# Performance work log

Hardware: AMD Instinct MI355X
Metric: run time of the kernel (lower is better)

Reference implementation:

```python
import jax, jax.numpy as jnp
from jax import lax
import numpy as np

EPS = 1e-5
K = 9  # 3x3 kernel points


def conv2d(x, w, b, pad, mode):
    if pad > 0:
        x = jnp.pad(x, ((0, 0), (0, 0), (pad, pad), (pad, pad)), mode=mode)
    y = lax.conv_general_dilated(x, w, (1, 1), 'VALID',
                                 dimension_numbers=('NCHW', 'OIHW', 'NCHW'))
    return y + b[None, :, None, None]


def inorm(x):
    m = jnp.mean(x, axis=(2, 3), keepdims=True)
    v = jnp.var(x, axis=(2, 3), keepdims=True)
    return (x - m) * lax.rsqrt(v + EPS)


def upsample2(x):
    return jnp.repeat(jnp.repeat(x, 2, axis=2), 2, axis=3)


def resblock(x, w1, b1, w2, b2):
    h = jax.nn.relu(inorm(conv2d(x, w1, b1, 1, 'reflect')))
    return x + inorm(conv2d(h, w2, b2, 1, 'reflect'))


def mod_deform_conv(feat, cat_in, w_off, b_off, w, b):
    # ModulatedDeformConvPack(double=True): offsets+mask predicted from cat_in
    # (2C channels), deformable 3x3 conv applied to feat (C channels).
    B, C, H, W = feat.shape
    om = conv2d(cat_in, w_off, b_off, 1, 'constant')          # [B, 3K, H, W]
    dy, dx = om[:, :K], om[:, K:2 * K]
    mask = jax.nn.sigmoid(om[:, 2 * K:])                       # [B, K, H, W]
    offset = jnp.concatenate([dy, dx], axis=1)                 # [B, 2K, H, W]
    ky = (jnp.arange(K) // 3 - 1).astype(feat.dtype)
    kx = (jnp.arange(K) % 3 - 1).astype(feat.dtype)
    py = jnp.arange(H, dtype=feat.dtype)[None, None, :, None] + ky[None, :, None, None] + dy
    px = jnp.arange(W, dtype=feat.dtype)[None, None, None, :] + kx[None, :, None, None] + dx
    y0 = jnp.floor(py); x0 = jnp.floor(px)
    wy = py - y0; wx = px - x0
    feat_flat = feat.reshape(B, C, H * W)

    def corner(yi, xi, wt):
        valid = (yi >= 0) & (yi < H) & (xi >= 0) & (xi < W)     # zero padding
        idx = (jnp.clip(yi, 0, H - 1).astype(jnp.int32) * W
               + jnp.clip(xi, 0, W - 1).astype(jnp.int32)).reshape(B, 1, K * H * W)
        g = jnp.take_along_axis(feat_flat, idx, axis=2).reshape(B, C, K, H, W)
        return g * (wt * valid)[:, None]

    val = (corner(y0, x0, (1 - wy) * (1 - wx)) + corner(y0, x0 + 1, (1 - wy) * wx)
           + corner(y0 + 1, x0, wy * (1 - wx)) + corner(y0 + 1, x0 + 1, wy * wx))
    val = val * mask[:, None]                                   # [B, C, K, H, W]
    out = jnp.einsum('bckhw,ock->bohw', val, w.reshape(w.shape[0], C, K))
    return out + b[None, :, None, None], offset


def decoder_forward(x, skip1, skip2,
                    rb1_w1, rb1_b1, rb1_w2, rb1_b2,
                    rb2_w1, rb2_b1, rb2_w2, rb2_b2,
                    c1_w, c1_b, c2_w, c2_b, c3_w, c3_b,
                    off2_w, off2_b, d2_w, d2_b,
                    off1_w, off1_b, d1_w, d1_b):
    out = resblock(x, rb1_w1, rb1_b1, rb1_w2, rb1_b2)           # i=0 ResBlocks
    out = resblock(out, rb2_w1, rb2_b1, rb2_w2, rb2_b2)
    out = upsample2(out)                                        # i=1
    out = jax.nn.relu(inorm(conv2d(out, c1_w, c1_b, 2, 'reflect')))  # i=2: [B,128,64,64]
    dcat = jnp.concatenate([out, skip2], axis=1)                # [B,256,64,64]
    cpre, offset2 = mod_deform_conv(skip2, dcat, off2_w, off2_b, d2_w, d2_b)
    out = jnp.concatenate([cpre, out], axis=1)                  # [B,256,64,64]
    out = upsample2(out)                                        # i=3
    out = jax.nn.relu(inorm(conv2d(out, c2_w, c2_b, 2, 'reflect')))  # i=4: [B,64,128,128]
    dcat = jnp.concatenate([out, skip1], axis=1)                # [B,128,128,128]
    cpre, offset1 = mod_deform_conv(skip1, dcat, off1_w, off1_b, d1_w, d1_b)
    out = jnp.concatenate([cpre, out], axis=1)                  # [B,128,128,128]
    out = jnp.tanh(conv2d(out, c3_w, c3_b, 3, 'reflect'))       # i=5: [B,3,128,128]
    offset_sum = (jnp.mean(jnp.abs(offset1)) + jnp.mean(jnp.abs(offset2))) / 2
    return out, offset_sum


def setup_inputs() -> dict:
    key = jax.random.key(0)
    ks = iter(jax.random.split(key, 32))

    def rn(shape, s):
        return jax.random.normal(next(ks), shape, dtype=jnp.float32) * s

    def wconv(shape):  # ~Kaiming-ish scale
        fan_in = shape[1] * shape[2] * shape[3]
        return rn(shape, 1.0 / np.sqrt(fan_in))

    inp = {
        'x': rn((4, 256, 32, 32), 1.0),
        'skip1': rn((4, 64, 128, 128), 1.0),
        'skip2': rn((4, 128, 64, 64), 1.0),
        'rb1_w1': wconv((256, 256, 3, 3)), 'rb1_b1': rn((256,), 0.01),
        'rb1_w2': wconv((256, 256, 3, 3)), 'rb1_b2': rn((256,), 0.01),
        'rb2_w1': wconv((256, 256, 3, 3)), 'rb2_b1': rn((256,), 0.01),
        'rb2_w2': wconv((256, 256, 3, 3)), 'rb2_b2': rn((256,), 0.01),
        'c1_w': wconv((128, 256, 5, 5)), 'c1_b': rn((128,), 0.01),
        'c2_w': wconv((64, 256, 5, 5)), 'c2_b': rn((64,), 0.01),
        'c3_w': wconv((3, 128, 7, 7)), 'c3_b': rn((3,), 0.01),
        'off2_w': rn((27, 256, 3, 3), 0.01), 'off2_b': rn((27,), 0.01),
        'd2_w': wconv((128, 128, 3, 3)), 'd2_b': rn((128,), 0.01),
        'off1_w': rn((27, 128, 3, 3), 0.01), 'off1_b': rn((27,), 0.01),
        'd1_w': wconv((64, 64, 3, 3)), 'd1_b': rn((64,), 0.01),
    }
    return inp


def reference(x, skip1, skip2,
              rb1_w1, rb1_b1, rb1_w2, rb1_b2,
              rb2_w1, rb2_b1, rb2_w2, rb2_b2,
              c1_w, c1_b, c2_w, c2_b, c3_w, c3_b,
              off2_w, off2_b, d2_w, d2_b,
              off1_w, off1_b, d1_w, d1_b):
    return decoder_forward(x, skip1, skip2,
                           rb1_w1, rb1_b1, rb1_w2, rb1_b2,
                           rb2_w1, rb2_b1, rb2_w2, rb2_b2,
                           c1_w, c1_b, c2_w, c2_b, c3_w, c3_b,
                           off2_w, off2_b, d2_w, d2_b,
                           off1_w, off1_b, d1_w, d1_b)
```

## Files before the change

kernel.cpp:

```cpp
#include <hip/hip_runtime.h>
#include <hip/hip_bf16.h>

#define DEV __device__ __forceinline__

typedef unsigned short u16;
typedef __attribute__((ext_vector_type(8))) short short8;
typedef __attribute__((ext_vector_type(4))) float float4v;

DEV u16 f2bf(float v) {
    __hip_bfloat16 h = __float2bfloat16(v);
    return *reinterpret_cast<u16*>(&h);
}
DEV float bf2f(u16 u) { return __uint_as_float(((unsigned)u) << 16); }

DEV float4v mfma16(short8 a, short8 b, float4v c) {
    return __builtin_amdgcn_mfma_f32_16x16x32_bf16(a, b, c, 0, 0, 0);
}

DEV void gload_lds16(const u16* g, u16* l) {
    __builtin_amdgcn_global_load_lds(
        (const __attribute__((address_space(1))) void*)g,
        (__attribute__((address_space(3))) void*)l, 16, 0, 0);
}

template <int K, bool UP, bool REFLECT, int NWO, int LGTW, int TH, int ACT = 0, int MF = 1>
__global__ __launch_bounds__(256) void mconv(
    const u16* __restrict__ X0, int c0ch,
    const u16* __restrict__ X1, int nch,
    const u16* __restrict__ WT, int NOB,
    const float* __restrict__ bias, float* __restrict__ out,
    int OC, int W, int H, int tilesX, int SW)
{
    constexpr int P    = (K - 1) / 2;
    constexpr int K2   = K * K;
    constexpr int NWP  = 4 / NWO;
    constexpr int TW   = 1 << LGTW;
    constexpr int LW   = TW + K - 1;
    constexpr int ROWS = TH + K - 1;
    constexpr int IT   = ROWS * LW;
    constexpr int ITP  = IT | 1;
    constexpr int ITEMS = ITP * 4;
    constexpr int CEIL = (ITEMS + 255) / 256;
    constexpr int BUF  = CEIL * 2048;

    extern __shared__ u16 Xs[];
    const int tid = threadIdx.x;
    const int wv = tid >> 6, lane = tid & 63, lm = lane & 15, lg = lane >> 4;
    const int wo = wv / NWP, wp = wv % NWP;
    const int bx = blockIdx.x, b = blockIdx.z;
    const int ty = bx / tilesX, tx = bx - ty * tilesX;
    const int row0 = ty * TH, col0 = tx * TW;
    const int SH  = UP ? (H >> 1) : H;
    const int HWs = SW * SH;
    const int obBase = blockIdx.y * (NWO * MF) + wo * MF;
    const int wbase = tid & 192;

    int offr[CEIL];
#pragma unroll
    for (int i = 0; i < CEIL; ++i) {
        int q = i * 256 + tid;
        bool bad = q >= ITEMS;
        if (bad) q = 0;
        int icg = q / ITP;
        int t   = q - icg * ITP;
        bad |= (t >= IT);
        int tr  = t / LW, tc = t - tr * LW;
        int gy = row0 - P + tr, gx = col0 - P + tc;
        if (REFLECT) {
            gy = gy < 0 ? -gy : (gy >= H ? 2 * H - 2 - gy : gy);
            gx = gx < 0 ? -gx : (gx >= W ? 2 * W - 2 - gx : gx);
            int sy = UP ? (gy >> 1) : gy, sx = UP ? (gx >> 1) : gx;
            offr[i] = bad ? -1 : (sy * SW + sx) * 32 + icg * 8;
        } else {
            bool ok = (gy >= 0) & (gy < H) & (gx >= 0) & (gx < W) & !bad;
            int sy = UP ? (gy >> 1) : gy, sx = UP ? (gx >> 1) : gx;
            offr[i] = ok ? (sy * SW + sx) * 32 + icg * 8 : -1;
        }
    }

    int rb16[4], opx[4];
#pragma unroll
    for (int nf = 0; nf < 4; ++nf) {
        int pt = wp * 64 + nf * 16 + lm;
        int ro = pt >> LGTW, co = pt & (TW - 1);
        rb16[nf] = (lg * ITP + ro * LW + co) * 8;
        opx[nf]  = (row0 + ro) * W + col0 + co;
    }

    float4v acc[MF][4];
#pragma unroll
    for (int m = 0; m < MF; ++m)
#pragma unroll
        for (int n = 0; n < 4; ++n) acc[m][n] = (float4v){0.f, 0.f, 0.f, 0.f};

    auto planeptr = [&](int ch) -> const u16* {
        return (ch < c0ch)
            ? X0 + (size_t)(b * c0ch + ch) * HWs * 32
            : X1 + (size_t)(b * (nch - c0ch) + (ch - c0ch)) * HWs * 32;
    };

    if (!REFLECT) {
        const uint4 UZ = {0u, 0u, 0u, 0u};
        for (int i = tid; i < BUF / 4; i += 256)
            *(uint4*)(Xs + (size_t)i * 8) = UZ;
        __syncthreads();
    }

    {
        const u16* src = planeptr(0);
#pragma unroll
        for (int i = 0; i < CEIL; ++i)
            if (offr[i] >= 0)
                gload_lds16(src + offr[i], &Xs[(size_t)(i * 256 + wbase) * 8]);
    }
    __syncthreads();

    int cur = 0;
    for (int ch = 0; ch < nch; ++ch) {
        if (ch + 1 < nch) {
            const u16* src = planeptr(ch + 1);
            u16* dstb = Xs + (size_t)(cur ^ 1) * BUF;
#pragma unroll
            for (int i = 0; i < CEIL; ++i)
                if (offr[i] >= 0)
                    gload_lds16(src + offr[i], &dstb[(size_t)(i * 256 + wbase) * 8]);
        }
        const u16* base = Xs + (size_t)cur * BUF;
        const u16* wch  = WT + ((size_t)ch * NOB + obBase) * K2 * 512 + lane * 8;
#pragma unroll
        for (int ky = 0; ky < K; ++ky) {
#pragma unroll
            for (int kx = 0; kx < K; ++kx) {
                const int tap = ky * K + kx;
                short8 Bf[4];
#pragma unroll
                for (int nf = 0; nf < 4; ++nf)
                    Bf[nf] = *(const short8*)(base + rb16[nf] + (ky * LW + kx) * 8);
#pragma unroll
                for (int m = 0; m < MF; ++m) {
                    short8 Af = *(const short8*)(wch + ((size_t)m * K2 + tap) * 512);
#pragma unroll
                    for (int nf = 0; nf < 4; ++nf)
                        acc[m][nf] = mfma16(Af, Bf[nf], acc[m][nf]);
                }
            }
        }
        __syncthreads();
        cur ^= 1;
    }

    const size_t HWo = (size_t)H * W;
#pragma unroll
    for (int m = 0; m < MF; ++m) {
        int oc0 = (obBase + m) * 16 + lg * 4;
#pragma unroll
        for (int nf = 0; nf < 4; ++nf) {
#pragma unroll
            for (int r = 0; r < 4; ++r) {
                int oc = oc0 + r;
                if (oc < OC) {
                    float v = acc[m][nf][r] + bias[oc];
                    if (ACT == 2) v = tanhf(v);
                    out[(size_t)(b * OC + oc) * HWo + opx[nf]] = v;
                }
            }
        }
    }
}

__global__ __launch_bounds__(256) void wtrans(
    const float* __restrict__ w, u16* __restrict__ wt,
    int OC, int IC, int K2, int NOB, int total)
{
    int i = blockIdx.x * 256 + threadIdx.x;
    if (i >= total) return;
    int e = i & 7;
    int l = (i >> 3) & 63;
    int rest = i >> 9;
    int tap = rest % K2;
    rest /= K2;
    int ob = rest % NOB;
    int ch = rest / NOB;
    int oc = ob * 16 + (l & 15);
    if (oc >= OC) oc = OC - 1;
    int ic = ch * 32 + (l >> 4) * 8 + e;
    wt[i] = f2bf(w[((size_t)oc * IC + ic) * K2 + tap]);
}

template <int C, int O>
__global__ __launch_bounds__(256) void dwtrans(
    const float* __restrict__ w, u16* __restrict__ dwt)
{
    constexpr int NOB = O / 16, NCC = C / 32;
    constexpr int total = 9 * NOB * NCC * 512;
    int i = blockIdx.x * 256 + threadIdx.x;
    if (i >= total) return;
    int e = i & 7;
    int l = (i >> 3) & 63;
    int rest = i >> 9;
    int cc = rest % NCC;
    rest /= NCC;
    int ob = rest % NOB;
    int k  = rest / NOB;
    int oc = ob * 16 + (l & 15);
    int ic = cc * 32 + (l >> 4) * 8 + e;
    dwt[i] = f2bf(w[((size_t)oc * C + ic) * 9 + k]);
}

template <int MODE, bool WF32>
__global__ __launch_bounds__(256) void pack32(
    const float* __restrict__ x, float* __restrict__ xout,
    const float* __restrict__ stats, const float* __restrict__ res,
    u16* __restrict__ tout, int lgHW, int lgC)
{
    __shared__ float tile[32][257];
    const int t   = threadIdx.x;
    const int px  = blockIdx.x * 256 + t;
    const int c0  = blockIdx.y * 32;
    const int b   = blockIdx.z;
    const int HW  = 1 << lgHW;
    const int C   = 1 << lgC;

#pragma unroll 8
    for (int c = 0; c < 32; ++c) {
        int bc = (b << lgC) + c0 + c;
        size_t idx = ((size_t)bc << lgHW) + px;
        float v = x[idx];
        if (MODE) {
            float m = stats[2 * bc], r = stats[2 * bc + 1];
            v = (v - m) * r;
            if (MODE == 1) v = fmaxf(v, 0.f);
            if (MODE == 2) v += res[idx];
        }
        if (WF32) xout[idx] = v;
        tile[c][t] = v;
    }
    __syncthreads();

    size_t o = ((((size_t)(b * (C >> 5) + (c0 >> 5)) << lgHW) + px) << 5);
#pragma unroll
    for (int g = 0; g < 4; ++g) {
        u16 tmp[8];
#pragma unroll
        for (int j = 0; j < 8; ++j)
            tmp[j] = f2bf(tile[g * 8 + j][t]);
        *(uint4*)(tout + o + g * 8) = *(const uint4*)tmp;
    }
}

__global__ __launch_bounds__(256) void inorm_stats(
    const float* __restrict__ x, float* __restrict__ stats, int HW)
{
    __shared__ float sh[8];
    const int bc = blockIdx.x;
    const float* p = x + (size_t)bc * HW;
    float s = 0.f, ss = 0.f;
    for (int i = threadIdx.x; i < HW; i += 256) {
        float v = p[i];
        s += v; ss = fmaf(v, v, ss);
    }
#pragma unroll
    for (int o = 32; o; o >>= 1) { s += __shfl_down(s, o); ss += __shfl_down(ss, o); }
    if ((threadIdx.x & 63) == 0) {
        sh[(threadIdx.x >> 6) * 2] = s;
        sh[(threadIdx.x >> 6) * 2 + 1] = ss;
    }
    __syncthreads();
    if (threadIdx.x == 0) {
        s  = sh[0] + sh[2] + sh[4] + sh[6];
        ss = sh[1] + sh[3] + sh[5] + sh[7];
        float m   = s / HW;
        float var = ss / HW - m * m;
        stats[2 * bc]     = m;
        stats[2 * bc + 1] = rsqrtf(var + 1e-5f);
    }
}

template <int C, int O, int MF>
__global__ __launch_bounds__(256) void deform_mfma(
    const u16* __restrict__ featT, const float* __restrict__ om,
    const u16* __restrict__ dwt, const float* __restrict__ bias,
    u16* __restrict__ outT, int H, int W, int lgW)
{
    constexpr int NOB = O / 16, NCC = C / 32;
    constexpr int NT = 576;
    constexpr int CPT = C / 4;
    const int HW = H * W;
    const int b  = blockIdx.y;
    const int p0 = blockIdx.x * 64;
    const int tid = threadIdx.x;
    const int wv = tid >> 6, lane = tid & 63, lm = lane & 15, lg = lane >> 4;

    __shared__ int   sO[4][NT];
    __shared__ float sW[4][NT];
    __shared__ u16   val[64 * C];

    for (int t = tid; t < NT; t += 256) {
        int px = t & 63, k = t >> 6;
        int p  = p0 + px;
        int hh = p >> lgW, ww = p & (W - 1);
        float dy = om[((size_t)b * 27 + k) * HW + p];
        float dx = om[((size_t)b * 27 + 9 + k) * HW + p];
        float mk = 1.f / (1.f + __expf(-om[((size_t)b * 27 + 18 + k) * HW + p]));
        float py  = (float)(hh + k / 3 - 1) + dy;
        float pxf = (float)(ww + k % 3 - 1) + dx;
        float y0f = floorf(py), x0f = floorf(pxf);
        int y0 = (int)y0f, x0 = (int)x0f;
        float wy = py - y0f, wx = pxf - x0f;
        float vy0 = ((unsigned)y0       < (unsigned)H) ? 1.f : 0.f;
        float vy1 = ((unsigned)(y0 + 1) < (unsigned)H) ? 1.f : 0.f;
        float vx0 = ((unsigned)x0       < (unsigned)W) ? 1.f : 0.f;
        float vx1 = ((unsigned)(x0 + 1) < (unsigned)W) ? 1.f : 0.f;
        int y0c = min(max(y0, 0), H - 1), y1c = min(max(y0 + 1, 0), H - 1);
        int x0c = min(max(x0, 0), W - 1), x1c = min(max(x0 + 1, 0), W - 1);
        sO[0][t] = y0c * W + x0c;  sO[1][t] = y0c * W + x1c;
        sO[2][t] = y1c * W + x0c;  sO[3][t] = y1c * W + x1c;
        sW[0][t] = (1.f - wy) * (1.f - wx) * vy0 * vx0 * mk;
        sW[1][t] = (1.f - wy) * wx         * vy0 * vx1 * mk;
        sW[2][t] = wy         * (1.f - wx) * vy1 * vx0 * mk;
        sW[3][t] = wy         * wx         * vy1 * vx1 * mk;
    }
    __syncthreads();

    float4v acc[MF][4];
#pragma unroll
    for (int m = 0; m < MF; ++m)
#pragma unroll
        for (int n = 0; n < 4; ++n) acc[m][n] = (float4v){0.f, 0.f, 0.f, 0.f};

    const int gpx = tid >> 2, gc0 = (tid & 3) * CPT;

    for (int k = 0; k < 9; ++k) {
        if (k) __syncthreads();
        {
            int t = k * 64 + gpx;
            int o0 = sO[0][t], o1 = sO[1][t], o2 = sO[2][t], o3 = sO[3][t];
            float w0 = sW[0][t], w1 = sW[1][t], w2 = sW[2][t], w3 = sW[3][t];
#pragma unroll
            for (int c8 = 0; c8 < CPT / 8; ++c8) {
                int c = gc0 + c8 * 8;
                const u16* base = featT + ((size_t)(b * NCC + (c >> 5)) * HW) * 32 + (c & 31);
                uint4 r0 = *(const uint4*)(base + (size_t)o0 * 32);
                uint4 r1 = *(const uint4*)(base + (size_t)o1 * 32);
                uint4 r2 = *(const uint4*)(base + (size_t)o2 * 32);
                uint4 r3 = *(const uint4*)(base + (size_t)o3 * 32);
                const u16* p0_ = (const u16*)&r0;
                const u16* p1_ = (const u16*)&r1;
                const u16* p2_ = (const u16*)&r2;
                const u16* p3_ = (const u16*)&r3;
                u16 outv[8];
#pragma unroll
                for (int j = 0; j < 8; ++j) {
                    float s = w0 * bf2f(p0_[j]) + w1 * bf2f(p1_[j])
                            + w2 * bf2f(p2_[j]) + w3 * bf2f(p3_[j]);
                    outv[j] = f2bf(s);
                }
                int csw = c ^ ((gpx & 7) << 3);
                *(uint4*)(val + gpx * C + csw) = *(uint4*)outv;
            }
        }
        __syncthreads();
        const u16* wk = dwt + (size_t)k * NOB * NCC * 512;
#pragma unroll
        for (int m = 0; m < MF; ++m) {
            int ob = wv * MF + m;
#pragma unroll
            for (int cc = 0; cc < NCC; ++cc) {
                short8 Af = *(const short8*)(wk + ((size_t)ob * NCC + cc) * 512 + lane * 8);
#pragma unroll
                for (int nf = 0; nf < 4; ++nf) {
                    int row = nf * 16 + lm;
                    int csw = (cc * 32 + lg * 8) ^ ((row & 7) << 3);
                    short8 Bf = *(const short8*)(val + row * C + csw);
                    acc[m][nf] = mfma16(Af, Bf, acc[m][nf]);
                }
            }
        }
    }

#pragma unroll
    for (int m = 0; m < MF; ++m) {
        int oc0 = (wv * MF + m) * 16 + lg * 4;
#pragma unroll
        for (int nf = 0; nf < 4; ++nf) {
            int p = p0 + nf * 16 + lm;
#pragma unroll
            for (int r = 0; r < 4; ++r) {
                int oc = oc0 + r;
                outT[((size_t)(b * (O / 32) + (oc >> 5)) * HW + p) * 32 + (oc & 31)]
                    = f2bf(acc[m][nf][r] + bias[oc]);
            }
        }
    }
}

__global__ __launch_bounds__(256) void absmean_partial(
    const float* __restrict__ om, int HW, float* __restrict__ partial)
{
    const int n18 = 18 * HW;
    const long long total = 4LL * n18;
    float s = 0.f;
    for (long long i = (long long)blockIdx.x * 256 + threadIdx.x; i < total;
         i += (long long)gridDim.x * 256) {
        int b = (int)(i / n18);
        int r = (int)(i % n18);
        s += fabsf(om[(size_t)b * 27 * HW + r]);
    }
    __shared__ float sh[4];
#pragma unroll
    for (int o = 32; o; o >>= 1) s += __shfl_down(s, o);
    if ((threadIdx.x & 63) == 0) sh[threadIdx.x >> 6] = s;
    __syncthreads();
    if (threadIdx.x == 0) partial[blockIdx.x] = sh[0] + sh[1] + sh[2] + sh[3];
}

__global__ __launch_bounds__(256) void finalize_k(
    const float* __restrict__ p1, const float* __restrict__ p2,
    float* __restrict__ outScalar)
{
    __shared__ float sh[8];
    float a = p1[threadIdx.x] + p1[threadIdx.x + 256];
    float b = p2[threadIdx.x] + p2[threadIdx.x + 256];
#pragma unroll
    for (int o = 32; o; o >>= 1) { a += __shfl_down(a, o); b += __shfl_down(b, o); }
    if ((threadIdx.x & 63) == 0) {
        sh[(threadIdx.x >> 6) * 2]     = a;
        sh[(threadIdx.x >> 6) * 2 + 1] = b;
    }
    __syncthreads();
    if (threadIdx.x == 0) {
        a = sh[0] + sh[2] + sh[4] + sh[6];
        b = sh[1] + sh[3] + sh[5] + sh[7];
        *outScalar = 0.5f * (a / (4.f * 18.f * 16384.f) + b / (4.f * 18.f * 4096.f));
    }
}

extern "C" void kernel_launch(void* const* d_in, const int* in_sizes, int n_in,
                              void* d_out, int out_size, void* d_ws, size_t ws_size,
                              hipStream_t stream)
{
    const float* x      = (const float*)d_in[0];
    const float* skip1  = (const float*)d_in[1];
    const float* skip2  = (const float*)d_in[2];
    const float* rb1_w1 = (const float*)d_in[3];
    const float* rb1_b1 = (const float*)d_in[4];
    const float* rb1_w2 = (const float*)d_in[5];
    const float* rb1_b2 = (const float*)d_in[6];
    const float* rb2_w1 = (const float*)d_in[7];
    const float* rb2_b1 = (const float*)d_in[8];
    const float* rb2_w2 = (const float*)d_in[9];
    const float* rb2_b2 = (const float*)d_in[10];
    const float* c1_w   = (const float*)d_in[11];
    const float* c1_b   = (const float*)d_in[12];
    const float* c2_w   = (const float*)d_in[13];
    const float* c2_b   = (const float*)d_in[14];
    const float* c3_w   = (const float*)d_in[15];
    const float* c3_b   = (const float*)d_in[16];
    const float* off2_w = (const float*)d_in[17];
    const float* off2_b = (const float*)d_in[18];
    const float* d2_w   = (const float*)d_in[19];
    const float* d2_b   = (const float*)d_in[20];
    const float* off1_w = (const float*)d_in[21];
    const float* off1_b = (const float*)d_in[22];
    const float* d1_w   = (const float*)d_in[23];
    const float* d1_b   = (const float*)d_in[24];

    float* ws    = (float*)d_ws;
    float* stats = ws;
    float* part2 = ws + 2048;
    float* part1 = ws + 2560;

    u16* wtRB = (u16*)(ws + 4096);
    u16* wtC1 = (u16*)(ws + 299008);
    u16* wtC2 = (u16*)(ws + 708608);
    u16* wtO2 = (u16*)(ws + 913408);
    u16* wtO1 = (u16*)(ws + 950272);
    float* R2  = ws + 968704;
    u16*  xT   = (u16*)(ws + 968704);
    u16*  A1T  = xT;
    u16*  A2T  = (u16*)(ws + 968704 + 524288);
    u16*  A3T  = A2T;
    float* A1  = ws + 968704 + 1048576;
    float* A2  = ws + 968704 + 2097152;
    float* A3  = ws + 968704 + 3145728;
    float* OM2 = ws + 968704;
    u16*  CP1T = (u16*)(ws + 968704);
    u16*  wtC3 = (u16*)(ws + 3065856);
    u16*  s1T  = (u16*)(ws + 5163008);
    float* R1  = ws + 7260160;
    u16*  wtD2 = (u16*)(ws + 7260160);
    u16*  CP2T = (u16*)(ws + 7333888);
    u16*  R2T  = (u16*)(ws + 7260160);
    u16*  R1T  = (u16*)(ws + 9357312);
    float* OM1 = ws + 9357312;
    u16*  s2T  = (u16*)(ws + 10405888);
    u16*  wtD1 = (u16*)(ws + 11126784);

    float* outp = (float*)d_out;
    dim3 blk(256);

    pack32<0, false><<<dim3(4, 8, 4), blk, 0, stream>>>(x, nullptr, nullptr, nullptr, xT, 10, 8);
    pack32<0, false><<<dim3(64, 2, 4), blk, 0, stream>>>(skip1, nullptr, nullptr, nullptr, s1T, 14, 6);
    pack32<0, false><<<dim3(16, 4, 4), blk, 0, stream>>>(skip2, nullptr, nullptr, nullptr, s2T, 12, 7);

    wtrans<<<2304, blk, 0, stream>>>(rb1_w1, wtRB, 256, 256, 9, 16, 589824);
    mconv<3, false, true, 2, 5, 4><<<dim3(8, 8, 4), blk, 32768, stream>>>(
        xT, 8, nullptr, 8, wtRB, 16, rb1_b1, A1, 256, 32, 32, 1, 32);
    inorm_stats<<<1024, blk, 0, stream>>>(A1, stats, 1024);
    pack32<1, false><<<dim3(4, 8, 4), blk, 0, stream>>>(A1, nullptr, stats, nullptr, A1T, 10, 8);
    wtrans<<<2304, blk, 0, stream>>>(rb1_w2, wtRB, 256, 256, 9, 16, 589824);
    mconv<3, false, true, 2, 5, 4><<<dim3(8, 8, 4), blk, 32768, stream>>>(
        A1T, 8, nullptr, 8, wtRB, 16, rb1_b2, A2, 256, 32, 32, 1, 32);
    inorm_stats<<<1024, blk, 0, stream>>>(A2, stats, 1024);
    pack32<2, true><<<dim3(4, 8, 4), blk, 0, stream>>>(A2, A2, stats, x, A2T, 10, 8);
    wtrans<<<2304, blk, 0, stream>>>(rb2_w1, wtRB, 256, 256, 9, 16, 589824);
    mconv<3, false, true, 2, 5, 4><<<dim3(8, 8, 4), blk, 32768, stream>>>(
        A2T, 8, nullptr, 8, wtRB, 16, rb2_b1, A1, 256, 32, 32, 1, 32);
    inorm_stats<<<1024, blk, 0, stream>>>(A1, stats, 1024);
    pack32<1, false><<<dim3(4, 8, 4), blk, 0, stream>>>(A1, nullptr, stats, nullptr, A1T, 10, 8);
    wtrans<<<2304, blk, 0, stream>>>(rb2_w2, wtRB, 256, 256, 9, 16, 589824);
    mconv<3, false, true, 2, 5, 4><<<dim3(8, 8, 4), blk, 32768, stream>>>(
        A1T, 8, nullptr, 8, wtRB, 16, rb2_b2, A3, 256, 32, 32, 1, 32);
    inorm_stats<<<1024, blk, 0, stream>>>(A3, stats, 1024);
    pack32<2, false><<<dim3(4, 8, 4), blk, 0, stream>>>(A3, nullptr, stats, A2, A3T, 10, 8);
    wtrans<<<3200, blk, 0, stream>>>(c1_w, wtC1, 128, 256, 25, 8, 819200);
    mconv<5, true, true, 2, 6, 2><<<dim3(32, 4, 4), blk, 57344, stream>>>(
        A3T, 8, nullptr, 8, wtC1, 8, c1_b, R1, 128, 64, 64, 1, 32);
    inorm_stats<<<512, blk, 0, stream>>>(R1, stats, 4096);
    pack32<1, false><<<dim3(16, 4, 4), blk, 0, stream>>>(R1, nullptr, stats, nullptr, R1T, 12, 7);
    wtrans<<<288, blk, 0, stream>>>(off2_w, wtO2, 27, 256, 9, 2, 73728);
    mconv<3, false, false, 2, 6, 2><<<dim3(32, 1, 4), blk, 40960, stream>>>(
        R1T, 4, s2T, 8, wtO2, 2, off2_b, OM2, 27, 64, 64, 1, 64);
    absmean_partial<<<512, blk, 0, stream>>>(OM2, 4096, part2);
    dwtrans<128, 128><<<576, blk, 0, stream>>>(d2_w, wtD2);
    deform_mfma<128, 128, 2><<<dim3(64, 4), blk, 0, stream>>>(
        s2T, OM2, wtD2, d2_b, CP2T, 64, 64, 6);
    wtrans<<<1600, blk, 0, stream>>>(c2_w, wtC2, 64, 256, 25, 4, 409600);
    mconv<5, true, true, 2, 6, 2, 0, 2><<<dim3(128, 1, 4), blk, 57344, stream>>>(
        CP2T, 4, R1T, 8, wtC2, 4, c2_b, R2, 64, 128, 128, 2, 64);
    inorm_stats<<<256, blk, 0, stream>>>(R2, stats, 16384);
    pack32<1, false><<<dim3(64, 2, 4), blk, 0, stream>>>(R2, nullptr, stats, nullptr, R2T, 14, 6);
    wtrans<<<144, blk, 0, stream>>>(off1_w, wtO1, 27, 128, 9, 2, 36864);
    mconv<3, false, false, 2, 6, 2><<<dim3(128, 1, 4), blk, 40960, stream>>>(
        R2T, 2, s1T, 4, wtO1, 2, off1_b, OM1, 27, 128, 128, 2, 128);
    absmean_partial<<<512, blk, 0, stream>>>(OM1, 16384, part1);
    dwtrans<64, 64><<<144, blk, 0, stream>>>(d1_w, wtD1);
    deform_mfma<64, 64, 1><<<dim3(256, 4), blk, 0, stream>>>(
        s1T, OM1, wtD1, d1_b, CP1T, 128, 128, 7);
    wtrans<<<392, blk, 0, stream>>>(c3_w, wtC3, 3, 128, 49, 1, 100352);
    mconv<7, false, true, 1, 4, 16, 2><<<dim3(64, 1, 4), blk, 65536, stream>>>(
        CP1T, 2, R2T, 4, wtC3, 1, c3_b, outp, 3, 128, 128, 8, 128);
    finalize_k<<<1, blk, 0, stream>>>(part1, part2, outp + 196608);
}
```

Baseline: 497.4 us.

## Split residual-block conv input channels across two blocks and batch weight packing

The four 256-channel 3x3 residual convs now split their input-channel loop into two halves along the z grid dimension. This doubles the block count from 256 to 512 to fill more compute units. Each half writes a partial sum to a separate buffer, and the following inorm_stats and pack32 kernels add the two partials on read. Five separate weight-transpose launches are merged into one batched launch at the start. The cost is extra fp32 partial writes and reads per resblock conv, and the workspace layout is shifted to make room for a relocated wtC3.

```diff
diff --git a/kernel.cpp b/kernel.cpp
--- a/kernel.cpp
+++ b/kernel.cpp
@@ -23,13 +23,15 @@
         (__attribute__((address_space(3))) void*)l, 16, 0, 0);
 }
 
-template <int K, bool UP, bool REFLECT, int NWO, int LGTW, int TH, int ACT = 0, int MF = 1>
+template <int K, bool UP, bool REFLECT, int NWO, int LGTW, int TH, int ACT = 0,
+          int MF = 1, int KSPLIT = 1>
 __global__ __launch_bounds__(256) void mconv(
     const u16* __restrict__ X0, int c0ch,
     const u16* __restrict__ X1, int nch,
     const u16* __restrict__ WT, int NOB,
     const float* __restrict__ bias, float* __restrict__ out,
-    int OC, int W, int H, int tilesX, int SW)
+    int OC, int W, int H, int tilesX, int SW,
+    float* __restrict__ outB = nullptr)
 {
     constexpr int P    = (K - 1) / 2;
     constexpr int K2   = K * K;
@@ -47,13 +49,18 @@
     const int tid = threadIdx.x;
     const int wv = tid >> 6, lane = tid & 63, lm = lane & 15, lg = lane >> 4;
     const int wo = wv / NWP, wp = wv % NWP;
-    const int bx = blockIdx.x, b = blockIdx.z;
+    const int bx = blockIdx.x;
+    const int bz = blockIdx.z;
+    const int b    = (KSPLIT == 1) ? bz : (bz >> 1);
+    const int half = (KSPLIT == 1) ? 0 : (bz & 1);
     const int ty = bx / tilesX, tx = bx - ty * tilesX;
     const int row0 = ty * TH, col0 = tx * TW;
     const int SH  = UP ? (H >> 1) : H;
     const int HWs = SW * SH;
     const int obBase = blockIdx.y * (NWO * MF) + wo * MF;
     const int wbase = tid & 192;
+    const int ch0 = half * (nch / KSPLIT);
+    const int ch1 = ch0 + nch / KSPLIT;
 
     int offr[CEIL];
 #pragma unroll
@@ -107,7 +114,7 @@
     }
 
     {
-        const u16* src = planeptr(0);
+        const u16* src = planeptr(ch0);
 #pragma unroll
         for (int i = 0; i < CEIL; ++i)
             if (offr[i] >= 0)
@@ -116,8 +123,8 @@
     __syncthreads();
 
     int cur = 0;
-    for (int ch = 0; ch < nch; ++ch) {
-        if (ch + 1 < nch) {
+    for (int ch = ch0; ch < ch1; ++ch) {
+        if (ch + 1 < ch1) {
             const u16* src = planeptr(ch + 1);
             u16* dstb = Xs + (size_t)(cur ^ 1) * BUF;
 #pragma unroll
@@ -150,6 +157,7 @@
     }
 
     const size_t HWo = (size_t)H * W;
+    float* dst = (KSPLIT == 2 && half) ? outB : out;
 #pragma unroll
     for (int m = 0; m < MF; ++m) {
         int oc0 = (obBase + m) * 16 + lg * 4;
@@ -159,21 +167,18 @@
             for (int r = 0; r < 4; ++r) {
                 int oc = oc0 + r;
                 if (oc < OC) {
-                    float v = acc[m][nf][r] + bias[oc];
+                    float bv = (KSPLIT == 2 && half) ? 0.f : bias[oc];
+                    float v = acc[m][nf][r] + bv;
                     if (ACT == 2) v = tanhf(v);
-                    out[(size_t)(b * OC + oc) * HWo + opx[nf]] = v;
+                    dst[(size_t)(b * OC + oc) * HWo + opx[nf]] = v;
                 }
             }
         }
     }
 }
 
-__global__ __launch_bounds__(256) void wtrans(
-    const float* __restrict__ w, u16* __restrict__ wt,
-    int OC, int IC, int K2, int NOB, int total)
-{
-    int i = blockIdx.x * 256 + threadIdx.x;
-    if (i >= total) return;
+DEV void wpack_one(const float* w, u16* wt, int OC, int IC, int K2, int NOB, int i)
+{
     int e = i & 7;
     int l = (i >> 3) & 63;
     int rest = i >> 9;
@@ -185,6 +190,28 @@
     if (oc >= OC) oc = OC - 1;
     int ic = ch * 32 + (l >> 4) * 8 + e;
     wt[i] = f2bf(w[((size_t)oc * IC + ic) * K2 + tap]);
+}
+
+__global__ __launch_bounds__(256) void wtrans(
+    const float* __restrict__ w, u16* __restrict__ wt,
+    int OC, int IC, int K2, int NOB, int total)
+{
+    int i = blockIdx.x * 256 + threadIdx.x;
+    if (i >= total) return;
+    wpack_one(w, wt, OC, IC, K2, NOB, i);
+}
+
+struct WSegs {
+    const float* w[5];
+    u16* dst[5];
+    int OC[5], IC[5], K2[5], NOB[5], total[5];
+};
+__global__ __launch_bounds__(256) void wpack_batch(WSegs s)
+{
+    int g = blockIdx.y;
+    int i = blockIdx.x * 256 + threadIdx.x;
+    if (i >= s.total[g]) return;
+    wpack_one(s.w[g], s.dst[g], s.OC[g], s.IC[g], s.K2[g], s.NOB[g], i);
 }
 
 template <int C, int O>
@@ -207,9 +234,10 @@
     dwt[i] = f2bf(w[((size_t)oc * C + ic) * 9 + k]);
 }
 
-template <int MODE, bool WF32>
+template <int MODE, bool WF32, bool ADD2 = false>
 __global__ __launch_bounds__(256) void pack32(
-    const float* __restrict__ x, float* __restrict__ xout,
+    const float* __restrict__ x, const float* __restrict__ x2,
+    float* __restrict__ xout,
     const float* __restrict__ stats, const float* __restrict__ res,
     u16* __restrict__ tout, int lgHW, int lgC)
 {
@@ -218,7 +246,6 @@
     const int px  = blockIdx.x * 256 + t;
     const int c0  = blockIdx.y * 32;
     const int b   = blockIdx.z;
-    const int HW  = 1 << lgHW;
     const int C   = 1 << lgC;
 
 #pragma unroll 8
@@ -226,6 +253,7 @@
         int bc = (b << lgC) + c0 + c;
         size_t idx = ((size_t)bc << lgHW) + px;
         float v = x[idx];
+        if (ADD2) v += x2[idx];
         if (MODE) {
             float m = stats[2 * bc], r = stats[2 * bc + 1];
             v = (v - m) * r;
@@ -249,14 +277,17 @@
 }
 
 __global__ __launch_bounds__(256) void inorm_stats(
-    const float* __restrict__ x, float* __restrict__ stats, int HW)
+    const float* __restrict__ x, const float* __restrict__ x2,
+    float* __restrict__ stats, int HW)
 {
     __shared__ float sh[8];
     const int bc = blockIdx.x;
-    const float* p = x + (size_t)bc * HW;
+    const float* p  = x + (size_t)bc * HW;
+    const float* p2 = x2 ? x2 + (size_t)bc * HW : nullptr;
     float s = 0.f, ss = 0.f;
     for (int i = threadIdx.x; i < HW; i += 256) {
         float v = p[i];
+        if (p2) v += p2[i];
         s += v; ss = fmaf(v, v, ss);
     }
 #pragma unroll
@@ -475,79 +506,82 @@
     u16* wtC2 = (u16*)(ws + 708608);
     u16* wtO2 = (u16*)(ws + 913408);
     u16* wtO1 = (u16*)(ws + 950272);
-    float* R2  = ws + 968704;
-    u16*  xT   = (u16*)(ws + 968704);
+    u16* wtC3 = (u16*)(ws + 968704);
+    float* R2  = ws + 1018880;
+    u16*  xT   = (u16*)(ws + 1018880);
     u16*  A1T  = xT;
-    u16*  A2T  = (u16*)(ws + 968704 + 524288);
+    u16*  A2T  = (u16*)(ws + 1018880 + 524288);
     u16*  A3T  = A2T;
-    float* A1  = ws + 968704 + 1048576;
-    float* A2  = ws + 968704 + 2097152;
-    float* A3  = ws + 968704 + 3145728;
-    float* OM2 = ws + 968704;
-    u16*  CP1T = (u16*)(ws + 968704);
-    u16*  wtC3 = (u16*)(ws + 3065856);
-    u16*  s1T  = (u16*)(ws + 5163008);
-    float* R1  = ws + 7260160;
-    u16*  wtD2 = (u16*)(ws + 7260160);
-    u16*  CP2T = (u16*)(ws + 7333888);
-    u16*  R2T  = (u16*)(ws + 7260160);
-    u16*  R1T  = (u16*)(ws + 9357312);
-    float* OM1 = ws + 9357312;
-    u16*  s2T  = (u16*)(ws + 10405888);
-    u16*  wtD1 = (u16*)(ws + 11126784);
+    float* A1  = ws + 1018880 + 1048576;
+    float* A2  = ws + 1018880 + 2097152;
+    float* A3  = ws + 1018880 + 3145728;
+    float* OM2 = ws + 1018880;
+    u16*  CP1T = (u16*)(ws + 1018880);
+    u16*  s1T  = (u16*)(ws + 5213184);
+    float* R1  = ws + 7310336;
+    u16*  wtD2 = (u16*)(ws + 7310336);
+    u16*  CP2T = (u16*)(ws + 7384064);
+    u16*  R2T  = (u16*)(ws + 7310336);
+    u16*  R1T  = (u16*)(ws + 9407488);
+    float* OM1 = ws + 9407488;
+    u16*  s2T  = (u16*)(ws + 10456064);
+    u16*  wtD1 = (u16*)(ws + 11176960);
 
     float* outp = (float*)d_out;
     dim3 blk(256);
 
-    pack32<0, false><<<dim3(4, 8, 4), blk, 0, stream>>>(x, nullptr, nullptr, nullptr, xT, 10, 8);
-    pack32<0, false><<<dim3(64, 2, 4), blk, 0, stream>>>(skip1, nullptr, nullptr, nullptr, s1T, 14, 6);
-    pack32<0, false><<<dim3(16, 4, 4), blk, 0, stream>>>(skip2, nullptr, nullptr, nullptr, s2T, 12, 7);
+    WSegs segs;
+    segs.w[0] = c1_w;  segs.dst[0] = wtC1; segs.OC[0] = 128; segs.IC[0] = 256; segs.K2[0] = 25; segs.NOB[0] = 8; segs.total[0] = 819200;
+    segs.w[1] = c2_w;  segs.dst[1] = wtC2; segs.OC[1] = 64;  segs.IC[1] = 256; segs.K2[1] = 25; segs.NOB[1] = 4; segs.total[1] = 409600;
+    segs.w[2] = off2_w; segs.dst[2] = wtO2; segs.OC[2] = 27; segs.IC[2] = 256; segs.K2[2] = 9;  segs.NOB[2] = 2; segs.total[2] = 73728;
+    segs.w[3] = off1_w; segs.dst[3] = wtO1; segs.OC[3] = 27; segs.IC[3] = 128; segs.K2[3] = 9;  segs.NOB[3] = 2; segs.total[3] = 36864;
+    segs.w[4] = c3_w;  segs.dst[4] = wtC3; segs.OC[4] = 3;   segs.IC[4] = 128; segs.K2[4] = 49; segs.NOB[4] = 1; segs.total[4] = 100352;
+    wpack_batch<<<dim3(3200, 5), blk, 0, stream>>>(segs);
+
+    pack32<0, false><<<dim3(4, 8, 4), blk, 0, stream>>>(x, nullptr, nullptr, nullptr, nullptr, xT, 10, 8);
+    pack32<0, false><<<dim3(64, 2, 4), blk, 0, stream>>>(skip1, nullptr, nullptr, nullptr, nullptr, s1T, 14, 6);
+    pack32<0, false><<<dim3(16, 4, 4), blk, 0, stream>>>(skip2, nullptr, nullptr, nullptr, nullptr, s2T, 12, 7);
 
     wtrans<<<2304, blk, 0, stream>>>(rb1_w1, wtRB, 256, 256, 9, 16, 589824);
-    mconv<3, false, true, 2, 5, 4><<<dim3(8, 8, 4), blk, 32768, stream>>>(
-        xT, 8, nullptr, 8, wtRB, 16, rb1_b1, A1, 256, 32, 32, 1, 32);
-    inorm_stats<<<1024, blk, 0, stream>>>(A1, stats, 1024);
-    pack32<1, false><<<dim3(4, 8, 4), blk, 0, stream>>>(A1, nullptr, stats, nullptr, A1T, 10, 8);
+    mconv<3, false, true, 2, 5, 4, 0, 1, 2><<<dim3(8, 8, 8), blk, 32768, stream>>>(
+        xT, 8, nullptr, 8, wtRB, 16, rb1_b1, A1, 256, 32, 32, 1, 32, A3);
+    inorm_stats<<<1024, blk, 0, stream>>>(A1, A3, stats, 1024);
+    pack32<1, false, true><<<dim3(4, 8, 4), blk, 0, stream>>>(A1, A3, nullptr, stats, nullptr, A1T, 10, 8);
     wtrans<<<2304, blk, 0, stream>>>(rb1_w2, wtRB, 256, 256, 9, 16, 589824);
-    mconv<3, false, true, 2, 5, 4><<<dim3(8, 8, 4), blk, 32768, stream>>>(
-        A1T, 8, nullptr, 8, wtRB, 16, rb1_b2, A2, 256, 32, 32, 1, 32);
-    inorm_stats<<<1024, blk, 0, stream>>>(A2, stats, 1024);
-    pack32<2, true><<<dim3(4, 8, 4), blk, 0, stream>>>(A2, A2, stats, x, A2T, 10, 8);
+    mconv<3, false, true, 2, 5, 4, 0, 1, 2><<<dim3(8, 8, 8), blk, 32768, stream>>>(
+        A1T, 8, nullptr, 8, wtRB, 16, rb1_b2, A2, 256, 32, 32, 1, 32, A3);
+    inorm_stats<<<1024, blk, 0, stream>>>(A2, A3, stats, 1024);
+    pack32<2, true, true><<<dim3(4, 8, 4), blk, 0, stream>>>(A2, A3, A2, stats, x, A2T, 10, 8);
     wtrans<<<2304, blk, 0, stream>>>(rb2_w1, wtRB, 256, 256, 9, 16, 589824);
-    mconv<3, false, true, 2, 5, 4><<<dim3(8, 8, 4), blk, 32768, stream>>>(
-        A2T, 8, nullptr, 8, wtRB, 16, rb2_b1, A1, 256, 32, 32, 1, 32);
-    inorm_stats<<<1024, blk, 0, stream>>>(A1, stats, 1024);
-    pack32<1, false><<<dim3(4, 8, 4), blk, 0, stream>>>(A1, nullptr, stats, nullptr, A1T, 10, 8);
+    mconv<3, false, true, 2, 5, 4, 0, 1, 2><<<dim3(8, 8, 8), blk, 32768, stream>>>(
+        A2T, 8, nullptr, 8, wtRB, 16, rb2_b1, A1, 256, 32, 32, 1, 32, A3);
+    inorm_stats<<<1024, blk, 0, stream>>>(A1, A3, stats, 1024);
+    pack32<1, false, true><<<dim3(4, 8, 4), blk, 0, stream>>>(A1, A3, nullptr, stats, nullptr, A1T, 10, 8);
     wtrans<<<2304, blk, 0, stream>>>(rb2_w2, wtRB, 256, 256, 9, 16, 589824);
-    mconv<3, false, true, 2, 5, 4><<<dim3(8, 8, 4), blk, 32768, stream>>>(
-        A1T, 8, nullptr, 8, wtRB, 16, rb2_b2, A3, 256, 32, 32, 1, 32);
-    inorm_stats<<<1024, blk, 0, stream>>>(A3, stats, 1024);
-    pack32<2, false><<<dim3(4, 8, 4), blk, 0, stream>>>(A3, nullptr, stats, A2, A3T, 10, 8);
-    wtrans<<<3200, blk, 0, stream>>>(c1_w, wtC1, 128, 256, 25, 8, 819200);
+    mconv<3, false, true, 2, 5, 4, 0, 1, 2><<<dim3(8, 8, 8), blk, 32768, stream>>>(
+        A1T, 8, nullptr, 8, wtRB, 16, rb2_b2, A3, 256, 32, 32, 1, 32, A1);
+    inorm_stats<<<1024, blk, 0, stream>>>(A3, A1, stats, 1024);
+    pack32<2, false, true><<<dim3(4, 8, 4), blk, 0, stream>>>(A3, A1, nullptr, stats, A2, A3T, 10, 8);
     mconv<5, true, true, 2, 6, 2><<<dim3(32, 4, 4), blk, 57344, stream>>>(
         A3T, 8, nullptr, 8, wtC1, 8, c1_b, R1, 128, 64, 64, 1, 32);
-    inorm_stats<<<512, blk, 0, stream>>>(R1, stats, 4096);
-    pack32<1, false><<<dim3(16, 4, 4), blk, 0, stream>>>(R1, nullptr, stats, nullptr, R1T, 12, 7);
-    wtrans<<<288, blk, 0, stream>>>(off2_w, wtO2, 27, 256, 9, 2, 73728);
+    inorm_stats<<<512, blk, 0, stream>>>(R1, nullptr, stats, 4096);
+    pack32<1, false><<<dim3(16, 4, 4), blk, 0, stream>>>(R1, nullptr, nullptr, stats, nullptr, R1T, 12, 7);
     mconv<3, false, false, 2, 6, 2><<<dim3(32, 1, 4), blk, 40960, stream>>>(
         R1T, 4, s2T, 8, wtO2, 2, off2_b, OM2, 27, 64, 64, 1, 64);
     absmean_partial<<<512, blk, 0, stream>>>(OM2, 4096, part2);
     dwtrans<128, 128><<<576, blk, 0, stream>>>(d2_w, wtD2);
     deform_mfma<128, 128, 2><<<dim3(64, 4), blk, 0, stream>>>(
         s2T, OM2, wtD2, d2_b, CP2T, 64, 64, 6);
-    wtrans<<<1600, blk, 0, stream>>>(c2_w, wtC2, 64, 256, 25, 4, 409600);
     mconv<5, true, true, 2, 6, 2, 0, 2><<<dim3(128, 1, 4), blk, 57344, stream>>>(
         CP2T, 4, R1T, 8, wtC2, 4, c2_b, R2, 64, 128, 128, 2, 64);
-    inorm_stats<<<256, blk, 0, stream>>>(R2, stats, 16384);
-    pack32<1, false><<<dim3(64, 2, 4), blk, 0, stream>>>(R2, nullptr, stats, nullptr, R2T, 14, 6);
-    wtrans<<<144, blk, 0, stream>>>(off1_w, wtO1, 27, 128, 9, 2, 36864);
+    inorm_stats<<<256, blk, 0, stream>>>(R2, nullptr, stats, 16384);
+    pack32<1, false><<<dim3(64, 2, 4), blk, 0, stream>>>(R2, nullptr, nullptr, stats, nullptr, R2T, 14, 6);
     mconv<3, false, false, 2, 6, 2><<<dim3(128, 1, 4), blk, 40960, stream>>>(
         R2T, 2, s1T, 4, wtO1, 2, off1_b, OM1, 27, 128, 128, 2, 128);
     absmean_partial<<<512, blk, 0, stream>>>(OM1, 16384, part1);
     dwtrans<64, 64><<<144, blk, 0, stream>>>(d1_w, wtD1);
     deform_mfma<64, 64, 1><<<dim3(256, 4), blk, 0, stream>>>(
         s1T, OM1, wtD1, d1_b, CP1T, 128, 128, 7);
-    wtrans<<<392, blk, 0, stream>>>(c3_w, wtC3, 3, 128, 49, 1, 100352);
     mconv<7, false, true, 1, 4, 16, 2><<<dim3(64, 1, 4), blk, 65536, stream>>>(
         CP1T, 2, R2T, 4, wtC3, 1, c3_b, outp, 3, 128, 128, 8, 128);
     finalize_k<<<1, blk, 0, stream>>>(part1, part2, outp + 196608);
```

Result: faster. 483.3 us (-2.8%).
